# Optimization experiments

Hardware: AMD Instinct MI355X
Metric: run time of the kernel (lower is better)

Reference implementation:

```python
import jax, jax.numpy as jnp
import numpy as np

B, N, C, H, E = 16, 512, 128, 8, 131072
Nn = B * N
Dh = C // H
EPS = 1e-5


def setup_inputs() -> dict:
    key = jax.random.key(0)
    ks = jax.random.split(key, 16)
    s = C ** -0.5
    x = jax.random.normal(ks[0], (Nn, C), dtype=jnp.float32)
    edge_index = jax.random.randint(ks[1], (2, E), 0, Nn)
    batch = jnp.arange(Nn) // N  # B equal-sized graphs, sorted
    attn_bias = jax.random.normal(ks[2], (B, N, N, H), dtype=jnp.float32)
    return {
        "x": x,
        "edge_index": edge_index,
        "batch": batch,
        "attn_bias": attn_bias,
        "conv_w": jax.random.normal(ks[3], (C, C)) * s,
        "conv_b": jnp.zeros((C,)),
        "wq": jax.random.normal(ks[4], (C, C)) * s,
        "bq": jnp.zeros((C,)),
        "wk": jax.random.normal(ks[5], (C, C)) * s,
        "bk": jnp.zeros((C,)),
        "wv": jax.random.normal(ks[6], (C, C)) * s,
        "bv": jnp.zeros((C,)),
        "wo": jax.random.normal(ks[7], (C, C)) * s,
        "bo": jnp.zeros((C,)),
        "w1": jax.random.normal(ks[8], (C, 2 * C)) * s,
        "b1": jnp.zeros((2 * C,)),
        "w2": jax.random.normal(ks[9], (2 * C, C)) * (2 * C) ** -0.5,
        "b2": jnp.zeros((C,)),
        "g1": jnp.ones((C,)), "be1": jnp.zeros((C,)),
        "g2": jnp.ones((C,)), "be2": jnp.zeros((C,)),
        "g3": jnp.ones((C,)), "be3": jnp.zeros((C,)),
    }


def _bn(h, g, b):
    # BatchNorm1d over the node dimension (training-mode batch statistics)
    mu = h.mean(axis=0)
    var = h.var(axis=0)  # biased, matches torch normalization
    return g * (h - mu) * jax.lax.rsqrt(var + EPS) + b


def reference(x, edge_index, batch, attn_bias,
              conv_w, conv_b, wq, bq, wk, bk, wv, bv, wo, bo,
              w1, b1, w2, b2, g1, be1, g2, be2, g3, be3):
    n_nodes, ch = x.shape
    bsz, n_max, _, heads = attn_bias.shape
    dh = ch // heads

    # ---- GCN conv (self loops + symmetric norm) -> dropout(0) + residual + norm1
    loops = jnp.arange(n_nodes)
    src = jnp.concatenate([edge_index[0], loops])
    dst = jnp.concatenate([edge_index[1], loops])
    deg = jax.ops.segment_sum(jnp.ones_like(src, dtype=x.dtype), dst, num_segments=n_nodes)
    dinv = jax.lax.rsqrt(jnp.maximum(deg, 1.0))
    xw = x @ conv_w
    msg = xw[src] * (dinv[src] * dinv[dst])[:, None]
    hconv = jax.ops.segment_sum(msg, dst, num_segments=n_nodes) + conv_b
    h1 = _bn(hconv + x, g1, be1)

    # ---- dense batch (equal-sized sorted graphs -> pure reshape, mask all-valid)
    xd = x.reshape(bsz, n_max, ch)
    q = ((xd @ wq + bq) * (dh ** -0.5)).reshape(bsz, n_max, heads, dh)
    k = (xd @ wk + bk).reshape(bsz, n_max, heads, dh)
    v = (xd @ wv + bv).reshape(bsz, n_max, heads, dh)
    scores = jnp.einsum('bqhd,bkhd->bqkh', q, k) + attn_bias  # [B,N,N,H]
    probs = jax.nn.softmax(scores, axis=2)
    att = jnp.einsum('bqkh,bkhd->bqhd', probs, v).reshape(bsz, n_max, ch)
    att = att @ wo + bo
    h2 = _bn(att.reshape(n_nodes, ch) + x, g2, be2)

    # ---- combine branches, MLP with residual, norm3
    out = h1 + h2
    mlp = jax.nn.relu(out @ w1 + b1) @ w2 + b2
    return _bn(out + mlp, g3, be3)
```

## Files before the change

kernel.cpp:

```cpp
#include <hip/hip_runtime.h>
#include <cstddef>

#define NN 8192
#define CC 128


__global__ __launch_bounds__(256) void count_deg_int_k(const int* __restrict__ dst, int* degi, int E) {
  int i = blockIdx.x * 256 + threadIdx.x;
  if (i < E) atomicAdd(&degi[dst[i]], 1);
}

__global__ __launch_bounds__(256) void dinv_k(const int* __restrict__ degi, float* __restrict__ dinv, int n) {
  int i = blockIdx.x * 256 + threadIdx.x;
  if (i < n) dinv[i] = rsqrtf((float)(degi[i] + 1));
}

__global__ __launch_bounds__(256) void scan_k(const int* __restrict__ degi, int* __restrict__ rowstart,
                                              int* __restrict__ cursor) {
  __shared__ int partial[256];
  int t = threadIdx.x;
  int base = t * 32;
  int local[32];
  int s = 0;
#pragma unroll
  for (int i = 0; i < 32; ++i) { local[i] = s; s += degi[base + i]; }
  partial[t] = s;
  __syncthreads();
  for (int off = 1; off < 256; off <<= 1) {
    int v = (t >= off) ? partial[t - off] : 0;
    __syncthreads();
    partial[t] += v;
    __syncthreads();
  }
  int offset = partial[t] - s;
#pragma unroll
  for (int i = 0; i < 32; ++i) {
    rowstart[base + i] = offset + local[i];
    cursor[base + i] = offset + local[i];
  }
  if (t == 255) rowstart[NN] = offset + s;
}

__global__ __launch_bounds__(256) void bucket_k(const int* __restrict__ src, const int* __restrict__ dst,
    int* __restrict__ cursor, int* __restrict__ col, int E) {
  int e = blockIdx.x * 256 + threadIdx.x;
  if (e >= E) return;
  int d = dst[e];
  int pos = atomicAdd(&cursor[d], 1);
  col[pos] = src[e];
}

__global__ __launch_bounds__(256) void gather_k(const int* __restrict__ rowstart, const int* __restrict__ col,
    const float* __restrict__ xw, const float* __restrict__ dinv, const float* __restrict__ cb,
    const float* __restrict__ x, float* __restrict__ h1) {
  int d = blockIdx.x * 2 + (threadIdx.x >> 7);
  int c = threadIdx.x & 127;
  int j0 = rowstart[d], j1 = rowstart[d + 1];
  float dd = dinv[d];
  float sum = 0.f;
  int s_next = (j0 < j1) ? col[j0] : 0;
  for (int j = j0; j < j1; ++j) {
    int s = s_next;
    if (j + 1 < j1) s_next = col[j + 1];
    sum += xw[(size_t)s * CC + c] * dinv[s];
  }
  sum *= dd;
  int idx = d * CC + c;
  sum += xw[idx] * dd * dd;
  h1[idx] = sum + cb[c] + x[idx];
}


__global__ __launch_bounds__(256) void bn_stats_k(const float* __restrict__ X,
    float* __restrict__ sums, float* __restrict__ sumsq) {
  int t = threadIdx.x;
  int c = t & 127, rg = t >> 7;
  int r0 = blockIdx.x * 64;
  float s = 0.f, sq = 0.f;
  for (int i = 0; i < 32; ++i) {
    float v = X[(size_t)(r0 + rg + 2 * i) * CC + c];
    s += v; sq += v * v;
  }
  atomicAdd(&sums[c], s);
  atomicAdd(&sumsq[c], sq);
}

__global__ void bn_finalize_k(const float* sums, const float* sumsq, const float* g, const float* be,
                              float* scale, float* shift) {
  int c = threadIdx.x;
  float mu = sums[c] * (1.0f / NN);
  float var = sumsq[c] * (1.0f / NN) - mu * mu;
  float sc = g[c] * rsqrtf(var + 1e-5f);
  scale[c] = sc;
  shift[c] = be[c] - mu * sc;
}

__global__ __launch_bounds__(256) void combine_k(const float* __restrict__ h1, const float* __restrict__ h2,
    const float* __restrict__ sc0, const float* __restrict__ sh0,
    const float* __restrict__ sc1, const float* __restrict__ sh1, float* __restrict__ out) {
  int idx = blockIdx.x * 256 + threadIdx.x;
  int c = idx & 127;
  out[idx] = sc0[c] * h1[idx] + sh0[c] + sc1[c] * h2[idx] + sh1[c];
}

__global__ __launch_bounds__(256) void bn_apply_k(const float* __restrict__ h, const float* __restrict__ sc,
    const float* __restrict__ sh, float* __restrict__ out) {
  int idx = blockIdx.x * 256 + threadIdx.x;
  int c = idx & 127;
  out[idx] = sc[c] * h[idx] + sh[c];
}

__global__ __launch_bounds__(256) void gemm_k(const float* __restrict__ A, const float* __restrict__ W,
    const float* __restrict__ bias, const float* __restrict__ resid, float* __restrict__ out,
    int M, int N, int K, float scale, int relu) {
  __shared__ float As[64 * 132];
  __shared__ float Ws[128 * 64];
  int t = threadIdx.x;
  int ty = t >> 4, tx = t & 15;
  int row0 = blockIdx.x * 64, n0 = blockIdx.y * 64;
  float acc[4][4] = {};
  for (int kc = 0; kc < K; kc += 128) {
#pragma unroll
    for (int j = 0; j < 8; ++j) {
      int f = t + 256 * j;
      int r = f >> 5, c4 = f & 31;
      *(float4*)(As + r * 132 + c4 * 4) = *(const float4*)(A + (size_t)(row0 + r) * K + kc + c4 * 4);
    }
#pragma unroll
    for (int j = 0; j < 8; ++j) {
      int f = t + 256 * j;
      int kr = f >> 4, c4 = f & 15;
      *(float4*)(Ws + kr * 64 + c4 * 4) = *(const float4*)(W + (size_t)(kc + kr) * N + n0 + c4 * 4);
    }
    __syncthreads();
    for (int k0 = 0; k0 < 128; k0 += 4) {
      float a[4][4], b[4][4];
#pragma unroll
      for (int i = 0; i < 4; ++i) {
        float4 t4 = *(const float4*)(As + (4 * ty + i) * 132 + k0);
        a[i][0] = t4.x; a[i][1] = t4.y; a[i][2] = t4.z; a[i][3] = t4.w;
      }
#pragma unroll
      for (int kk = 0; kk < 4; ++kk) {
        float4 t4 = *(const float4*)(Ws + (k0 + kk) * 64 + 4 * tx);
        b[kk][0] = t4.x; b[kk][1] = t4.y; b[kk][2] = t4.z; b[kk][3] = t4.w;
      }
#pragma unroll
      for (int kk = 0; kk < 4; ++kk)
#pragma unroll
        for (int i = 0; i < 4; ++i)
#pragma unroll
          for (int j = 0; j < 4; ++j)
            acc[i][j] += a[i][kk] * b[kk][j];
    }
    __syncthreads();
  }
  float4 bv = make_float4(0.f, 0.f, 0.f, 0.f);
  if (bias) bv = *(const float4*)(bias + n0 + 4 * tx);
#pragma unroll
  for (int i = 0; i < 4; ++i) {
    float4 r;
    r.x = (acc[i][0] + bv.x) * scale;
    r.y = (acc[i][1] + bv.y) * scale;
    r.z = (acc[i][2] + bv.z) * scale;
    r.w = (acc[i][3] + bv.w) * scale;
    if (relu) { r.x = fmaxf(r.x, 0.f); r.y = fmaxf(r.y, 0.f); r.z = fmaxf(r.z, 0.f); r.w = fmaxf(r.w, 0.f); }
    size_t o = (size_t)(row0 + 4 * ty + i) * N + n0 + 4 * tx;
    if (resid) {
      float4 rv = *(const float4*)(resid + o);
      r.x += rv.x; r.y += rv.y; r.z += rv.z; r.w += rv.w;
    }
    *(float4*)(out + o) = r;
  }
}

#define ROWS 160
__global__ __launch_bounds__(128) void attn_k(const float* __restrict__ Q, const float* __restrict__ K,
    const float* __restrict__ V, const float* __restrict__ bias,
    float* __restrict__ accA, float* __restrict__ accB, float* __restrict__ ml) {
  __shared__ float Ks[64 * ROWS];
  __shared__ float Vs[64 * ROWS];
  const int t = threadIdx.x;
  const int b = blockIdx.x >> 4;
  const int qt = blockIdx.x & 15;
  const int s = blockIdx.y;
  const int qp = t >> 3;
  const int h = t & 7;
  const int node0 = b * 512 + qt * 32 + qp * 2;

  float qf0[16], qf1[16];
  {
    const float4* qa = (const float4*)(Q + (size_t)node0 * CC + h * 16);
    const float4* qb = (const float4*)(Q + (size_t)(node0 + 1) * CC + h * 16);
#pragma unroll
    for (int i = 0; i < 4; ++i) {
      float4 a = qa[i], c = qb[i];
      qf0[4*i] = a.x; qf0[4*i+1] = a.y; qf0[4*i+2] = a.z; qf0[4*i+3] = a.w;
      qf1[4*i] = c.x; qf1[4*i+1] = c.y; qf1[4*i+2] = c.z; qf1[4*i+3] = c.w;
    }
  }
  float m0 = -INFINITY, l0 = 0.f, m1 = -INFINITY, l1 = 0.f;
  float ac0[16], ac1[16];
#pragma unroll
  for (int d = 0; d < 16; ++d) { ac0[d] = 0.f; ac1[d] = 0.f; }

  const float* brow0 = bias + (size_t)node0 * 4096 + h;
  const float* brow1 = brow0 + 4096;
  const int kbase0 = s * 256;
  float b0c[8], b1c[8], b0n[8], b1n[8];
#pragma unroll
  for (int j = 0; j < 8; ++j) {
    b0c[j] = brow0[(size_t)(kbase0 + j) * 8];
    b1c[j] = brow1[(size_t)(kbase0 + j) * 8];
  }

  const size_t kvbase = (size_t)b * 512 * CC + (size_t)kbase0 * CC;
  for (int kt = 0; kt < 4; ++kt) {
    __syncthreads();
#pragma unroll
    for (int j = 0; j < 16; ++j) {
      int f = t + 128 * j;
      int r = f >> 5, c4 = f & 31;
      int lo = r * ROWS + (c4 >> 2) * 20 + (c4 & 3) * 4;
      size_t go = kvbase + (size_t)(kt * 64 + r) * CC + c4 * 4;
      *(float4*)(Ks + lo) = *(const float4*)(K + go);
      *(float4*)(Vs + lo) = *(const float4*)(V + go);
    }
    __syncthreads();
    for (int c = 0; c < 8; ++c) {
      int lc = kt * 8 + c;
      if (lc < 31) {
#pragma unroll
        for (int j = 0; j < 8; ++j) {
          size_t o = (size_t)(kbase0 + (lc + 1) * 8 + j) * 8;
          b0n[j] = brow0[o];
          b1n[j] = brow1[o];
        }
      }
#pragma unroll
      for (int j = 0; j < 8; ++j) {
        int kk = c * 8 + j;
        const float4* kf = (const float4*)(Ks + kk * ROWS + h * 20);
        float4 k0 = kf[0], k1 = kf[1], k2 = kf[2], k3 = kf[3];
        float kv[16] = {k0.x,k0.y,k0.z,k0.w,k1.x,k1.y,k1.z,k1.w,
                        k2.x,k2.y,k2.z,k2.w,k3.x,k3.y,k3.z,k3.w};
        float s0 = b0c[j], s1 = b1c[j];
#pragma unroll
        for (int d = 0; d < 16; ++d) { s0 += qf0[d] * kv[d]; s1 += qf1[d] * kv[d]; }
        if (s0 > m0) {
          float al = __expf(m0 - s0);
          l0 *= al;
#pragma unroll
          for (int d = 0; d < 16; ++d) ac0[d] *= al;
          m0 = s0;
        }
        if (s1 > m1) {
          float al = __expf(m1 - s1);
          l1 *= al;
#pragma unroll
          for (int d = 0; d < 16; ++d) ac1[d] *= al;
          m1 = s1;
        }
        float p0 = __expf(s0 - m0);
        float p1 = __expf(s1 - m1);
        l0 += p0; l1 += p1;
        const float4* vf = (const float4*)(Vs + kk * ROWS + h * 20);
        float4 v0 = vf[0], v1 = vf[1], v2 = vf[2], v3 = vf[3];
        float vv[16] = {v0.x,v0.y,v0.z,v0.w,v1.x,v1.y,v1.z,v1.w,
                        v2.x,v2.y,v2.z,v2.w,v3.x,v3.y,v3.z,v3.w};
#pragma unroll
        for (int d = 0; d < 16; ++d) { ac0[d] += p0 * vv[d]; ac1[d] += p1 * vv[d]; }
      }
#pragma unroll
      for (int j = 0; j < 8; ++j) { b0c[j] = b0n[j]; b1c[j] = b1n[j]; }
    }
  }
  float* dst = s ? accB : accA;
  float* o0 = dst + (size_t)node0 * CC + h * 16;
  float* o1 = o0 + CC;
#pragma unroll
  for (int i = 0; i < 4; ++i) {
    *(float4*)(o0 + 4 * i) = make_float4(ac0[4*i], ac0[4*i+1], ac0[4*i+2], ac0[4*i+3]);
    *(float4*)(o1 + 4 * i) = make_float4(ac1[4*i], ac1[4*i+1], ac1[4*i+2], ac1[4*i+3]);
  }
  float* mlp = ml + (size_t)s * 65536 * 2;
  int i0 = (node0 * 8 + h) * 2;
  mlp[i0] = m0; mlp[i0 + 1] = l0;
  mlp[i0 + 16] = m1; mlp[i0 + 17] = l1;
}

__global__ __launch_bounds__(256) void attn_merge_k(const float* __restrict__ accA, const float* __restrict__ accB,
    const float* __restrict__ ml, float* __restrict__ out) {
  int i = blockIdx.x * 256 + threadIdx.x;
  int node = i >> 3, h = i & 7;
  float m0 = ml[i * 2], l0 = ml[i * 2 + 1];
  float m1 = ml[131072 + i * 2], l1 = ml[131072 + i * 2 + 1];
  float M = fmaxf(m0, m1);
  float a0 = __expf(m0 - M), a1 = __expf(m1 - M);
  float inv = 1.f / (l0 * a0 + l1 * a1);
  a0 *= inv; a1 *= inv;
  const float4* pa = (const float4*)(accA + (size_t)node * CC + h * 16);
  const float4* pb = (const float4*)(accB + (size_t)node * CC + h * 16);
  float4* po = (float4*)(out + (size_t)node * CC + h * 16);
#pragma unroll
  for (int k = 0; k < 4; ++k) {
    float4 x = pa[k], y = pb[k];
    po[k] = make_float4(x.x * a0 + y.x * a1, x.y * a0 + y.y * a1,
                        x.z * a0 + y.z * a1, x.w * a0 + y.w * a1);
  }
}


extern "C" void kernel_launch(void* const* d_in, const int* in_sizes, int n_in,
                              void* d_out, int out_size, void* d_ws, size_t ws_size,
                              hipStream_t stream) {
  const float* x      = (const float*)d_in[0];
  const int*   ei     = (const int*)d_in[1];
  const float* bias   = (const float*)d_in[3];
  const float* conv_w = (const float*)d_in[4];
  const float* conv_b = (const float*)d_in[5];
  const float* wq = (const float*)d_in[6];
  const float* bq = (const float*)d_in[7];
  const float* wk = (const float*)d_in[8];
  const float* bk = (const float*)d_in[9];
  const float* wv = (const float*)d_in[10];
  const float* bv = (const float*)d_in[11];
  const float* wo = (const float*)d_in[12];
  const float* bo = (const float*)d_in[13];
  const float* w1 = (const float*)d_in[14];
  const float* b1 = (const float*)d_in[15];
  const float* w2 = (const float*)d_in[16];
  const float* b2 = (const float*)d_in[17];
  const float* g1 = (const float*)d_in[18];
  const float* be1 = (const float*)d_in[19];
  const float* g2 = (const float*)d_in[20];
  const float* be2 = (const float*)d_in[21];
  const float* g3 = (const float*)d_in[22];
  const float* be3 = (const float*)d_in[23];
  int E = in_sizes[1] / 2;

  float* ws = (float*)d_ws;
  const size_t NC = (size_t)NN * CC;
  float* xw     = ws;
  float* h1pre  = ws + NC;
  float* qb     = ws + 2 * NC;
  float* kb     = ws + 3 * NC;
  float* vb     = ws + 4 * NC;
  float* h2pre  = ws + 5 * NC;
  float* outbuf = ws + 6 * NC;
  float* hid    = ws + 2 * NC;
  float* h3pre  = ws + 4 * NC;
  float* st     = ws + 7 * NC;
  float* dinv   = ws + 7 * NC + 1536;
  int*   degi     = (int*)(ws + 7 * NC + 1536 + NN);
  int*   rowstart = degi + NN;
  int*   cursor   = rowstart + NN + 1;
  int*   col      = cursor + NN;
  float* mlbuf    = (float*)(col + E);

  hipMemsetAsync(degi, 0, NN * sizeof(int), stream);
  hipMemsetAsync(st, 0, 1536 * sizeof(float), stream);

  count_deg_int_k<<<(E + 255) / 256, 256, 0, stream>>>(ei + E, degi, E);
  dinv_k<<<NN / 256, 256, 0, stream>>>(degi, dinv, NN);
  scan_k<<<1, 256, 0, stream>>>(degi, rowstart, cursor);
  bucket_k<<<(E + 255) / 256, 256, 0, stream>>>(ei, ei + E, cursor, col, E);
  gemm_k<<<dim3(NN / 64, 2), 256, 0, stream>>>(x, conv_w, nullptr, nullptr, xw, NN, CC, CC, 1.f, 0);
  gather_k<<<NN / 2, 256, 0, stream>>>(rowstart, col, xw, dinv, conv_b, x, h1pre);
  bn_stats_k<<<NN / 64, 256, 0, stream>>>(h1pre, st + 0, st + 128);

  gemm_k<<<dim3(NN / 64, 2), 256, 0, stream>>>(x, wq, bq, nullptr, qb, NN, CC, CC, 0.25f, 0);
  gemm_k<<<dim3(NN / 64, 2), 256, 0, stream>>>(x, wk, bk, nullptr, kb, NN, CC, CC, 1.f, 0);
  gemm_k<<<dim3(NN / 64, 2), 256, 0, stream>>>(x, wv, bv, nullptr, vb, NN, CC, CC, 1.f, 0);
  attn_k<<<dim3(256, 2), 128, 0, stream>>>(qb, kb, vb, bias, h2pre, outbuf, mlbuf);
  attn_merge_k<<<65536 / 256, 256, 0, stream>>>(h2pre, outbuf, mlbuf, xw);
  gemm_k<<<dim3(NN / 64, 2), 256, 0, stream>>>(xw, wo, bo, x, h2pre, NN, CC, CC, 1.f, 0);
  bn_stats_k<<<NN / 64, 256, 0, stream>>>(h2pre, st + 256, st + 384);

  bn_finalize_k<<<1, 128, 0, stream>>>(st + 0, st + 128, g1, be1, st + 768, st + 896);
  bn_finalize_k<<<1, 128, 0, stream>>>(st + 256, st + 384, g2, be2, st + 1024, st + 1152);
  combine_k<<<NC / 256, 256, 0, stream>>>(h1pre, h2pre, st + 768, st + 896, st + 1024, st + 1152, outbuf);
  gemm_k<<<dim3(NN / 64, 4), 256, 0, stream>>>(outbuf, w1, b1, nullptr, hid, NN, 2 * CC, CC, 1.f, 1);
  gemm_k<<<dim3(NN / 64, 2), 256, 0, stream>>>(hid, w2, b2, outbuf, h3pre, NN, CC, 2 * CC, 1.f, 0);
  bn_stats_k<<<NN / 64, 256, 0, stream>>>(h3pre, st + 512, st + 640);
  bn_finalize_k<<<1, 128, 0, stream>>>(st + 512, st + 640, g3, be3, st + 1280, st + 1408);
  bn_apply_k<<<NC / 256, 256, 0, stream>>>(h3pre, st + 1280, st + 1408, (float*)d_out);
}
```

Before: 452.2 us.

## Split attention into four key chunks with bf16 partials and fold BN finalize

The attention kernel now splits keys into four 128-key chunks with 64-thread blocks, each thread handling four query rows, and stores partial accumulators as packed bf16 for a four-way merge. The GCN degree scaling moves into the xw GEMM epilogue so the gather loop skips per-edge dinv loads, and the BN finalize kernels are folded into combine/apply. The aim is more parallel blocks for attention and fewer launches and loads. Storing partials in bf16 loses precision, and the smaller K tiles mean more sync steps.

```diff
diff --git a/kernel.cpp b/kernel.cpp
--- a/kernel.cpp
+++ b/kernel.cpp
@@ -3,6 +3,16 @@
 
 #define NN 8192
 #define CC 128
+
+static __device__ inline unsigned f2bf_pack(float a, float b) {
+  unsigned ua = __builtin_bit_cast(unsigned, a);
+  ua += 0x7fffu + ((ua >> 16) & 1u);
+  unsigned ub = __builtin_bit_cast(unsigned, b);
+  ub += 0x7fffu + ((ub >> 16) & 1u);
+  return (ua >> 16) | (ub & 0xffff0000u);
+}
+static __device__ inline float bf_lo(unsigned u) { return __builtin_bit_cast(float, u << 16); }
+static __device__ inline float bf_hi(unsigned u) { return __builtin_bit_cast(float, u & 0xffff0000u); }
 
 
 __global__ __launch_bounds__(256) void count_deg_int_k(const int* __restrict__ dst, int* degi, int E) {
@@ -51,23 +61,24 @@
 }
 
 __global__ __launch_bounds__(256) void gather_k(const int* __restrict__ rowstart, const int* __restrict__ col,
-    const float* __restrict__ xw, const float* __restrict__ dinv, const float* __restrict__ cb,
+    const float* __restrict__ xws, const float* __restrict__ dinv, const float* __restrict__ cb,
     const float* __restrict__ x, float* __restrict__ h1) {
   int d = blockIdx.x * 2 + (threadIdx.x >> 7);
   int c = threadIdx.x & 127;
   int j0 = rowstart[d], j1 = rowstart[d + 1];
   float dd = dinv[d];
   float sum = 0.f;
-  int s_next = (j0 < j1) ? col[j0] : 0;
+  float v = 0.f;
+  if (j0 < j1) v = xws[(size_t)col[j0] * CC + c];
   for (int j = j0; j < j1; ++j) {
-    int s = s_next;
-    if (j + 1 < j1) s_next = col[j + 1];
-    sum += xw[(size_t)s * CC + c] * dinv[s];
-  }
-  sum *= dd;
+    float v_next = 0.f;
+    if (j + 1 < j1) v_next = xws[(size_t)col[j + 1] * CC + c];
+    sum += v;
+    v = v_next;
+  }
   int idx = d * CC + c;
-  sum += xw[idx] * dd * dd;
-  h1[idx] = sum + cb[c] + x[idx];
+  sum += xws[idx];
+  h1[idx] = sum * dd + cb[c] + x[idx];
 }
 
 
@@ -85,34 +96,36 @@
   atomicAdd(&sumsq[c], sq);
 }
 
-__global__ void bn_finalize_k(const float* sums, const float* sumsq, const float* g, const float* be,
-                              float* scale, float* shift) {
-  int c = threadIdx.x;
-  float mu = sums[c] * (1.0f / NN);
-  float var = sumsq[c] * (1.0f / NN) - mu * mu;
-  float sc = g[c] * rsqrtf(var + 1e-5f);
-  scale[c] = sc;
-  shift[c] = be[c] - mu * sc;
-}
-
 __global__ __launch_bounds__(256) void combine_k(const float* __restrict__ h1, const float* __restrict__ h2,
-    const float* __restrict__ sc0, const float* __restrict__ sh0,
-    const float* __restrict__ sc1, const float* __restrict__ sh1, float* __restrict__ out) {
+    const float* __restrict__ st, const float* __restrict__ g1, const float* __restrict__ be1,
+    const float* __restrict__ g2, const float* __restrict__ be2, float* __restrict__ out) {
   int idx = blockIdx.x * 256 + threadIdx.x;
   int c = idx & 127;
-  out[idx] = sc0[c] * h1[idx] + sh0[c] + sc1[c] * h2[idx] + sh1[c];
-}
-
-__global__ __launch_bounds__(256) void bn_apply_k(const float* __restrict__ h, const float* __restrict__ sc,
-    const float* __restrict__ sh, float* __restrict__ out) {
+  float mu1 = st[c] * (1.f / NN);
+  float var1 = st[128 + c] * (1.f / NN) - mu1 * mu1;
+  float sc1 = g1[c] * rsqrtf(var1 + 1e-5f);
+  float sh1 = be1[c] - mu1 * sc1;
+  float mu2 = st[256 + c] * (1.f / NN);
+  float var2 = st[384 + c] * (1.f / NN) - mu2 * mu2;
+  float sc2 = g2[c] * rsqrtf(var2 + 1e-5f);
+  float sh2 = be2[c] - mu2 * sc2;
+  out[idx] = sc1 * h1[idx] + sh1 + sc2 * h2[idx] + sh2;
+}
+
+__global__ __launch_bounds__(256) void bn_apply_k(const float* __restrict__ h, const float* __restrict__ st,
+    const float* __restrict__ g3, const float* __restrict__ be3, float* __restrict__ out) {
   int idx = blockIdx.x * 256 + threadIdx.x;
   int c = idx & 127;
-  out[idx] = sc[c] * h[idx] + sh[c];
+  float mu = st[512 + c] * (1.f / NN);
+  float var = st[640 + c] * (1.f / NN) - mu * mu;
+  float sc = g3[c] * rsqrtf(var + 1e-5f);
+  float sh = be3[c] - mu * sc;
+  out[idx] = sc * h[idx] + sh;
 }
 
 __global__ __launch_bounds__(256) void gemm_k(const float* __restrict__ A, const float* __restrict__ W,
-    const float* __restrict__ bias, const float* __restrict__ resid, float* __restrict__ out,
-    int M, int N, int K, float scale, int relu) {
+    const float* __restrict__ bias, const float* __restrict__ resid, const float* __restrict__ dscale,
+    float* __restrict__ out, int M, int N, int K, float scale, int relu) {
   __shared__ float As[64 * 132];
   __shared__ float Ws[128 * 64];
   int t = threadIdx.x;
@@ -159,13 +172,15 @@
   if (bias) bv = *(const float4*)(bias + n0 + 4 * tx);
 #pragma unroll
   for (int i = 0; i < 4; ++i) {
+    int row = row0 + 4 * ty + i;
+    float ds = dscale ? dscale[row] : 1.f;
     float4 r;
-    r.x = (acc[i][0] + bv.x) * scale;
-    r.y = (acc[i][1] + bv.y) * scale;
-    r.z = (acc[i][2] + bv.z) * scale;
-    r.w = (acc[i][3] + bv.w) * scale;
+    r.x = (acc[i][0] + bv.x) * scale * ds;
+    r.y = (acc[i][1] + bv.y) * scale * ds;
+    r.z = (acc[i][2] + bv.z) * scale * ds;
+    r.w = (acc[i][3] + bv.w) * scale * ds;
     if (relu) { r.x = fmaxf(r.x, 0.f); r.y = fmaxf(r.y, 0.f); r.z = fmaxf(r.z, 0.f); r.w = fmaxf(r.w, 0.f); }
-    size_t o = (size_t)(row0 + 4 * ty + i) * N + n0 + 4 * tx;
+    size_t o = (size_t)row * N + n0 + 4 * tx;
     if (resid) {
       float4 rv = *(const float4*)(resid + o);
       r.x += rv.x; r.y += rv.y; r.z += rv.z; r.w += rv.w;
@@ -175,139 +190,148 @@
 }
 
 #define ROWS 160
-__global__ __launch_bounds__(128) void attn_k(const float* __restrict__ Q, const float* __restrict__ K,
+__global__ __launch_bounds__(64, 2) void attn_k(const float* __restrict__ Q, const float* __restrict__ K,
     const float* __restrict__ V, const float* __restrict__ bias,
-    float* __restrict__ accA, float* __restrict__ accB, float* __restrict__ ml) {
-  __shared__ float Ks[64 * ROWS];
-  __shared__ float Vs[64 * ROWS];
+    unsigned* __restrict__ pA, unsigned* __restrict__ pB, float* __restrict__ ml) {
+  __shared__ float Ks[16 * ROWS];
+  __shared__ float Vs[16 * ROWS];
   const int t = threadIdx.x;
   const int b = blockIdx.x >> 4;
   const int qt = blockIdx.x & 15;
   const int s = blockIdx.y;
-  const int qp = t >> 3;
+  const int qq = t >> 3;
   const int h = t & 7;
-  const int node0 = b * 512 + qt * 32 + qp * 2;
-
-  float qf0[16], qf1[16];
-  {
-    const float4* qa = (const float4*)(Q + (size_t)node0 * CC + h * 16);
-    const float4* qb = (const float4*)(Q + (size_t)(node0 + 1) * CC + h * 16);
+  const int node0 = b * 512 + qt * 32 + qq * 4;
+
+  float qf[4][16];
+#pragma unroll
+  for (int r = 0; r < 4; ++r) {
+    const float4* qp = (const float4*)(Q + (size_t)(node0 + r) * CC + h * 16);
 #pragma unroll
     for (int i = 0; i < 4; ++i) {
-      float4 a = qa[i], c = qb[i];
-      qf0[4*i] = a.x; qf0[4*i+1] = a.y; qf0[4*i+2] = a.z; qf0[4*i+3] = a.w;
-      qf1[4*i] = c.x; qf1[4*i+1] = c.y; qf1[4*i+2] = c.z; qf1[4*i+3] = c.w;
-    }
-  }
-  float m0 = -INFINITY, l0 = 0.f, m1 = -INFINITY, l1 = 0.f;
-  float ac0[16], ac1[16];
-#pragma unroll
-  for (int d = 0; d < 16; ++d) { ac0[d] = 0.f; ac1[d] = 0.f; }
-
-  const float* brow0 = bias + (size_t)node0 * 4096 + h;
-  const float* brow1 = brow0 + 4096;
-  const int kbase0 = s * 256;
-  float b0c[8], b1c[8], b0n[8], b1n[8];
-#pragma unroll
-  for (int j = 0; j < 8; ++j) {
-    b0c[j] = brow0[(size_t)(kbase0 + j) * 8];
-    b1c[j] = brow1[(size_t)(kbase0 + j) * 8];
-  }
-
-  const size_t kvbase = (size_t)b * 512 * CC + (size_t)kbase0 * CC;
-  for (int kt = 0; kt < 4; ++kt) {
-    __syncthreads();
-#pragma unroll
-    for (int j = 0; j < 16; ++j) {
-      int f = t + 128 * j;
+      float4 a = qp[i];
+      qf[r][4*i] = a.x; qf[r][4*i+1] = a.y; qf[r][4*i+2] = a.z; qf[r][4*i+3] = a.w;
+    }
+  }
+  float m[4], l[4], acc[4][16];
+#pragma unroll
+  for (int r = 0; r < 4; ++r) {
+    m[r] = -INFINITY; l[r] = 0.f;
+#pragma unroll
+    for (int d = 0; d < 16; ++d) acc[r][d] = 0.f;
+  }
+
+  const float* bbase = bias + (size_t)node0 * 4096 + (size_t)s * 128 * 8 + h;
+  float bc[4], b1[4], b2[4];
+#pragma unroll
+  for (int r = 0; r < 4; ++r) {
+    bc[r] = bbase[(size_t)r * 4096 + 0 * 8];
+    b1[r] = bbase[(size_t)r * 4096 + 1 * 8];
+    b2[r] = bbase[(size_t)r * 4096 + 2 * 8];
+  }
+
+  const size_t kvbase = (size_t)b * 512 * CC + (size_t)s * 128 * CC;
+  for (int kt = 0; kt < 8; ++kt) {
+    __syncthreads();
+#pragma unroll
+    for (int j = 0; j < 8; ++j) {
+      int f = t + 64 * j;
       int r = f >> 5, c4 = f & 31;
       int lo = r * ROWS + (c4 >> 2) * 20 + (c4 & 3) * 4;
-      size_t go = kvbase + (size_t)(kt * 64 + r) * CC + c4 * 4;
+      size_t go = kvbase + (size_t)(kt * 16 + r) * CC + c4 * 4;
       *(float4*)(Ks + lo) = *(const float4*)(K + go);
       *(float4*)(Vs + lo) = *(const float4*)(V + go);
     }
     __syncthreads();
-    for (int c = 0; c < 8; ++c) {
-      int lc = kt * 8 + c;
-      if (lc < 31) {
-#pragma unroll
-        for (int j = 0; j < 8; ++j) {
-          size_t o = (size_t)(kbase0 + (lc + 1) * 8 + j) * 8;
-          b0n[j] = brow0[o];
-          b1n[j] = brow1[o];
+#pragma unroll 4
+    for (int kk = 0; kk < 16; ++kk) {
+      int key = kt * 16 + kk;
+      const float4* kf = (const float4*)(Ks + kk * ROWS + h * 20);
+      float4 k0 = kf[0], k1 = kf[1], k2 = kf[2], k3 = kf[3];
+      float kv[16] = {k0.x,k0.y,k0.z,k0.w,k1.x,k1.y,k1.z,k1.w,
+                      k2.x,k2.y,k2.z,k2.w,k3.x,k3.y,k3.z,k3.w};
+      const float4* vf = (const float4*)(Vs + kk * ROWS + h * 20);
+      float4 v0 = vf[0], v1 = vf[1], v2 = vf[2], v3 = vf[3];
+      float vv[16] = {v0.x,v0.y,v0.z,v0.w,v1.x,v1.y,v1.z,v1.w,
+                      v2.x,v2.y,v2.z,v2.w,v3.x,v3.y,v3.z,v3.w};
+#pragma unroll
+      for (int r = 0; r < 4; ++r) {
+        float sc = bc[r];
+#pragma unroll
+        for (int d = 0; d < 16; ++d) sc += qf[r][d] * kv[d];
+        if (sc > m[r]) {
+          float al = __expf(m[r] - sc);
+          l[r] *= al;
+#pragma unroll
+          for (int d = 0; d < 16; ++d) acc[r][d] *= al;
+          m[r] = sc;
         }
+        float p = __expf(sc - m[r]);
+        l[r] += p;
+#pragma unroll
+        for (int d = 0; d < 16; ++d) acc[r][d] += p * vv[d];
       }
 #pragma unroll
-      for (int j = 0; j < 8; ++j) {
-        int kk = c * 8 + j;
-        const float4* kf = (const float4*)(Ks + kk * ROWS + h * 20);
-        float4 k0 = kf[0], k1 = kf[1], k2 = kf[2], k3 = kf[3];
-        float kv[16] = {k0.x,k0.y,k0.z,k0.w,k1.x,k1.y,k1.z,k1.w,
-                        k2.x,k2.y,k2.z,k2.w,k3.x,k3.y,k3.z,k3.w};
-        float s0 = b0c[j], s1 = b1c[j];
-#pragma unroll
-        for (int d = 0; d < 16; ++d) { s0 += qf0[d] * kv[d]; s1 += qf1[d] * kv[d]; }
-        if (s0 > m0) {
-          float al = __expf(m0 - s0);
-          l0 *= al;
-#pragma unroll
-          for (int d = 0; d < 16; ++d) ac0[d] *= al;
-          m0 = s0;
-        }
-        if (s1 > m1) {
-          float al = __expf(m1 - s1);
-          l1 *= al;
-#pragma unroll
-          for (int d = 0; d < 16; ++d) ac1[d] *= al;
-          m1 = s1;
-        }
-        float p0 = __expf(s0 - m0);
-        float p1 = __expf(s1 - m1);
-        l0 += p0; l1 += p1;
-        const float4* vf = (const float4*)(Vs + kk * ROWS + h * 20);
-        float4 v0 = vf[0], v1 = vf[1], v2 = vf[2], v3 = vf[3];
-        float vv[16] = {v0.x,v0.y,v0.z,v0.w,v1.x,v1.y,v1.z,v1.w,
-                        v2.x,v2.y,v2.z,v2.w,v3.x,v3.y,v3.z,v3.w};
-#pragma unroll
-        for (int d = 0; d < 16; ++d) { ac0[d] += p0 * vv[d]; ac1[d] += p1 * vv[d]; }
+      for (int r = 0; r < 4; ++r) { bc[r] = b1[r]; b1[r] = b2[r]; }
+      int nk = key + 3;
+      if (nk < 128) {
+#pragma unroll
+        for (int r = 0; r < 4; ++r) b2[r] = bbase[(size_t)r * 4096 + (size_t)nk * 8];
       }
-#pragma unroll
-      for (int j = 0; j < 8; ++j) { b0c[j] = b0n[j]; b1c[j] = b1n[j]; }
-    }
-  }
-  float* dst = s ? accB : accA;
-  float* o0 = dst + (size_t)node0 * CC + h * 16;
-  float* o1 = o0 + CC;
-#pragma unroll
-  for (int i = 0; i < 4; ++i) {
-    *(float4*)(o0 + 4 * i) = make_float4(ac0[4*i], ac0[4*i+1], ac0[4*i+2], ac0[4*i+3]);
-    *(float4*)(o1 + 4 * i) = make_float4(ac1[4*i], ac1[4*i+1], ac1[4*i+2], ac1[4*i+3]);
-  }
-  float* mlp = ml + (size_t)s * 65536 * 2;
-  int i0 = (node0 * 8 + h) * 2;
-  mlp[i0] = m0; mlp[i0 + 1] = l0;
-  mlp[i0 + 16] = m1; mlp[i0 + 17] = l1;
-}
-
-__global__ __launch_bounds__(256) void attn_merge_k(const float* __restrict__ accA, const float* __restrict__ accB,
-    const float* __restrict__ ml, float* __restrict__ out) {
+    }
+  }
+
+  unsigned* pbase = (s < 2 ? pA : pB) + (size_t)(s & 1) * (NN * CC / 2);
+#pragma unroll
+  for (int r = 0; r < 4; ++r) {
+    int slot = ((node0 + r) * 8 + h) * 8;
+    unsigned u[8];
+#pragma unroll
+    for (int j = 0; j < 8; ++j) u[j] = f2bf_pack(acc[r][2*j], acc[r][2*j+1]);
+    *(uint4*)(pbase + slot)     = make_uint4(u[0], u[1], u[2], u[3]);
+    *(uint4*)(pbase + slot + 4) = make_uint4(u[4], u[5], u[6], u[7]);
+    int mi = (s * 65536 + (node0 + r) * 8 + h) * 2;
+    ml[mi] = m[r]; ml[mi + 1] = l[r];
+  }
+}
+
+__global__ __launch_bounds__(256) void attn_merge_k(const unsigned* __restrict__ pA,
+    const unsigned* __restrict__ pB, const float* __restrict__ ml, float* __restrict__ out) {
   int i = blockIdx.x * 256 + threadIdx.x;
-  int node = i >> 3, h = i & 7;
-  float m0 = ml[i * 2], l0 = ml[i * 2 + 1];
-  float m1 = ml[131072 + i * 2], l1 = ml[131072 + i * 2 + 1];
-  float M = fmaxf(m0, m1);
-  float a0 = __expf(m0 - M), a1 = __expf(m1 - M);
-  float inv = 1.f / (l0 * a0 + l1 * a1);
-  a0 *= inv; a1 *= inv;
-  const float4* pa = (const float4*)(accA + (size_t)node * CC + h * 16);
-  const float4* pb = (const float4*)(accB + (size_t)node * CC + h * 16);
-  float4* po = (float4*)(out + (size_t)node * CC + h * 16);
-#pragma unroll
-  for (int k = 0; k < 4; ++k) {
-    float4 x = pa[k], y = pb[k];
-    po[k] = make_float4(x.x * a0 + y.x * a1, x.y * a0 + y.y * a1,
-                        x.z * a0 + y.z * a1, x.w * a0 + y.w * a1);
-  }
+  float ms[4], ls[4];
+  float M = -INFINITY;
+#pragma unroll
+  for (int s = 0; s < 4; ++s) {
+    ms[s] = ml[(s * 65536 + i) * 2];
+    ls[s] = ml[(s * 65536 + i) * 2 + 1];
+    M = fmaxf(M, ms[s]);
+  }
+  float w[4], L = 0.f;
+#pragma unroll
+  for (int s = 0; s < 4; ++s) { w[s] = __expf(ms[s] - M); L += ls[s] * w[s]; }
+  float inv = 1.f / L;
+#pragma unroll
+  for (int s = 0; s < 4; ++s) w[s] *= inv;
+
+  float o[16];
+#pragma unroll
+  for (int d = 0; d < 16; ++d) o[d] = 0.f;
+#pragma unroll
+  for (int s = 0; s < 4; ++s) {
+    const unsigned* pb = (s < 2 ? pA : pB) + (size_t)(s & 1) * (NN * CC / 2) + (size_t)i * 8;
+    uint4 a = *(const uint4*)pb;
+    uint4 b = *(const uint4*)(pb + 4);
+    unsigned u[8] = {a.x, a.y, a.z, a.w, b.x, b.y, b.z, b.w};
+#pragma unroll
+    for (int j = 0; j < 8; ++j) {
+      o[2*j]   += w[s] * bf_lo(u[j]);
+      o[2*j+1] += w[s] * bf_hi(u[j]);
+    }
+  }
+  float* po = out + (size_t)i * 16;
+#pragma unroll
+  for (int j = 0; j < 4; ++j)
+    *(float4*)(po + 4 * j) = make_float4(o[4*j], o[4*j+1], o[4*j+2], o[4*j+3]);
 }
 
 
@@ -351,38 +375,35 @@
   float* hid    = ws + 2 * NC;
   float* h3pre  = ws + 4 * NC;
   float* st     = ws + 7 * NC;
-  float* dinv   = ws + 7 * NC + 1536;
-  int*   degi     = (int*)(ws + 7 * NC + 1536 + NN);
+  float* dinv   = ws + 7 * NC + 768;
+  int*   degi     = (int*)(ws + 7 * NC + 768 + NN);
   int*   rowstart = degi + NN;
   int*   cursor   = rowstart + NN + 1;
   int*   col      = cursor + NN;
   float* mlbuf    = (float*)(col + E);
 
   hipMemsetAsync(degi, 0, NN * sizeof(int), stream);
-  hipMemsetAsync(st, 0, 1536 * sizeof(float), stream);
+  hipMemsetAsync(st, 0, 768 * sizeof(float), stream);
 
   count_deg_int_k<<<(E + 255) / 256, 256, 0, stream>>>(ei + E, degi, E);
   dinv_k<<<NN / 256, 256, 0, stream>>>(degi, dinv, NN);
   scan_k<<<1, 256, 0, stream>>>(degi, rowstart, cursor);
   bucket_k<<<(E + 255) / 256, 256, 0, stream>>>(ei, ei + E, cursor, col, E);
-  gemm_k<<<dim3(NN / 64, 2), 256, 0, stream>>>(x, conv_w, nullptr, nullptr, xw, NN, CC, CC, 1.f, 0);
+  gemm_k<<<dim3(NN / 64, 2), 256, 0, stream>>>(x, conv_w, nullptr, nullptr, dinv, xw, NN, CC, CC, 1.f, 0);
   gather_k<<<NN / 2, 256, 0, stream>>>(rowstart, col, xw, dinv, conv_b, x, h1pre);
   bn_stats_k<<<NN / 64, 256, 0, stream>>>(h1pre, st + 0, st + 128);
 
-  gemm_k<<<dim3(NN / 64, 2), 256, 0, stream>>>(x, wq, bq, nullptr, qb, NN, CC, CC, 0.25f, 0);
-  gemm_k<<<dim3(NN / 64, 2), 256, 0, stream>>>(x, wk, bk, nullptr, kb, NN, CC, CC, 1.f, 0);
-  gemm_k<<<dim3(NN / 64, 2), 256, 0, stream>>>(x, wv, bv, nullptr, vb, NN, CC, CC, 1.f, 0);
-  attn_k<<<dim3(256, 2), 128, 0, stream>>>(qb, kb, vb, bias, h2pre, outbuf, mlbuf);
-  attn_merge_k<<<65536 / 256, 256, 0, stream>>>(h2pre, outbuf, mlbuf, xw);
-  gemm_k<<<dim3(NN / 64, 2), 256, 0, stream>>>(xw, wo, bo, x, h2pre, NN, CC, CC, 1.f, 0);
+  gemm_k<<<dim3(NN / 64, 2), 256, 0, stream>>>(x, wq, bq, nullptr, nullptr, qb, NN, CC, CC, 0.25f, 0);
+  gemm_k<<<dim3(NN / 64, 2), 256, 0, stream>>>(x, wk, bk, nullptr, nullptr, kb, NN, CC, CC, 1.f, 0);
+  gemm_k<<<dim3(NN / 64, 2), 256, 0, stream>>>(x, wv, bv, nullptr, nullptr, vb, NN, CC, CC, 1.f, 0);
+  attn_k<<<dim3(256, 4), 64, 0, stream>>>(qb, kb, vb, bias, (unsigned*)xw, (unsigned*)h2pre, mlbuf);
+  attn_merge_k<<<65536 / 256, 256, 0, stream>>>((unsigned*)xw, (unsigned*)h2pre, mlbuf, outbuf);
+  gemm_k<<<dim3(NN / 64, 2), 256, 0, stream>>>(outbuf, wo, bo, x, nullptr, h2pre, NN, CC, CC, 1.f, 0);
   bn_stats_k<<<NN / 64, 256, 0, stream>>>(h2pre, st + 256, st + 384);
 
-  bn_finalize_k<<<1, 128, 0, stream>>>(st + 0, st + 128, g1, be1, st + 768, st + 896);
-  bn_finalize_k<<<1, 128, 0, stream>>>(st + 256, st + 384, g2, be2, st + 1024, st + 1152);
-  combine_k<<<NC / 256, 256, 0, stream>>>(h1pre, h2pre, st + 768, st + 896, st + 1024, st + 1152, outbuf);
-  gemm_k<<<dim3(NN / 64, 4), 256, 0, stream>>>(outbuf, w1, b1, nullptr, hid, NN, 2 * CC, CC, 1.f, 1);
-  gemm_k<<<dim3(NN / 64, 2), 256, 0, stream>>>(hid, w2, b2, outbuf, h3pre, NN, CC, 2 * CC, 1.f, 0);
+  combine_k<<<NC / 256, 256, 0, stream>>>(h1pre, h2pre, st, g1, be1, g2, be2, outbuf);
+  gemm_k<<<dim3(NN / 64, 4), 256, 0, stream>>>(outbuf, w1, b1, nullptr, nullptr, hid, NN, 2 * CC, CC, 1.f, 1);
+  gemm_k<<<dim3(NN / 64, 2), 256, 0, stream>>>(hid, w2, b2, outbuf, nullptr, h3pre, NN, CC, 2 * CC, 1.f, 0);
   bn_stats_k<<<NN / 64, 256, 0, stream>>>(h3pre, st + 512, st + 640);
-  bn_finalize_k<<<1, 128, 0, stream>>>(st + 512, st + 640, g3, be3, st + 1280, st + 1408);
-  bn_apply_k<<<NC / 256, 256, 0, stream>>>(h3pre, st + 1280, st + 1408, (float*)d_out);
-}
+  bn_apply_k<<<NC / 256, 256, 0, stream>>>(h3pre, st, g3, be3, (float*)d_out);
+}
```

Result: slower. 467.9 us (+3.5%).
